# Optimization experiments

Measured on AMD Instinct MI355X. Metric: run time of the kernel, lower is better.

The kernel has to match this reference:

```python
import jax, jax.numpy as jnp
import numpy as np

B, T, E, H = 1, 4096, 768, 12
DH = E // H


def setup_inputs() -> dict:
    key = jax.random.key(0)
    ks = jax.random.split(key, 10)
    s = 0.02
    inp = {
        "queries": jax.random.normal(ks[0], (B, T, E), jnp.float32),
        "values": jax.random.normal(ks[1], (B, T, E), jnp.float32),
        # causal mask (1 = keep, 0 = masked), matches masked_fill(mask == 0, -1e9)
        "mask": jnp.tril(jnp.ones((T, T), jnp.int32))[None, None, :, :],
        "Wq": jax.random.normal(ks[2], (E, E), jnp.float32) * s,
        "bq": jnp.zeros((E,), jnp.float32),
        "Wk": jax.random.normal(ks[3], (E, E), jnp.float32) * s,
        "bk": jnp.zeros((E,), jnp.float32),
        "Wv": jax.random.normal(ks[4], (E, E), jnp.float32) * s,
        "bv": jnp.zeros((E,), jnp.float32),
        "Wo": jax.random.normal(ks[5], (E, E), jnp.float32) * s,
        "bo": jnp.zeros((E,), jnp.float32),
    }
    return inp


def _split_heads(x):
    # [B,T,E] -> [B,H,T,DH]
    return x.reshape(B, T, H, DH).transpose(0, 2, 1, 3)


def reference(queries, values, mask, Wq, bq, Wk, bk, Wv, bv, Wo, bo):
    # torch nn.Linear: y = x @ W.T + b
    q = _split_heads(queries @ Wq.T + bq)
    k = _split_heads(values @ Wk.T + bk)
    v = _split_heads(values @ Wv.T + bv)
    scale = 1.0 / np.sqrt(DH).astype(np.float32)
    logits = jnp.einsum("bhqd,bhkd->bhqk", q, k) * scale  # [B,H,T,T]
    logits = jnp.where(mask == 0, jnp.float32(-1e9), logits)
    probs = jax.nn.softmax(logits, axis=-1)
    ctx = jnp.einsum("bhqk,bhkd->bhqd", probs, v)  # [B,H,T,DH]
    ctx = ctx.transpose(0, 2, 1, 3).reshape(B, T, E)
    return ctx @ Wo.T + bo
```

## Files before the change

kernel.cpp:

```cpp
#include <hip/hip_runtime.h>
#include <hip/hip_bf16.h>


typedef __hip_bfloat16 bf16;
typedef __attribute__((ext_vector_type(8))) short short8;
typedef __attribute__((ext_vector_type(4))) short short4v;
typedef __attribute__((ext_vector_type(4))) float f32x4;

#define TSEQ 4096
#define NHEAD 12
#define DHEAD 64
#define EMB 768

#if defined(__HIP_DEVICE_COMPILE__)
#define MFMA16(a, b, c) __builtin_amdgcn_mfma_f32_16x16x16bf16_1k(a, b, c, 0, 0, 0)
#else
#define MFMA16(a, b, c) (c)
#endif

typedef const __attribute__((address_space(1))) unsigned int* gptr_t;
typedef __attribute__((address_space(3))) unsigned int* lptr_t;

__device__ __forceinline__ void load_lds16(const void* g, void* l) {
    __builtin_amdgcn_global_load_lds((gptr_t)g, (lptr_t)l, 16, 0, 0);
}

__device__ __forceinline__ float b2f(short s) {
    unsigned u = ((unsigned)(unsigned short)s) << 16;
    float f;
    __builtin_memcpy(&f, &u, 4);
    return f;
}

__device__ __forceinline__ short f2bs(float f) {
    bf16 h = __float2bfloat16(f);
    short s;
    __builtin_memcpy(&s, &h, 2);
    return s;
}

struct CvtJob { const float* src; bf16* dst; int n; };
struct CvtArgs { CvtJob j[6]; };

__global__ __launch_bounds__(256) void cvt_kernel(CvtArgs a) {
    const CvtJob jb = a.j[blockIdx.y];
    const int i = (blockIdx.x * 256 + threadIdx.x) * 8;
    if (i >= jb.n) return;
    const float4 x0 = *(const float4*)(jb.src + i);
    const float4 x1 = *(const float4*)(jb.src + i + 4);
    bf16 tmp[8];
    tmp[0] = __float2bfloat16(x0.x); tmp[1] = __float2bfloat16(x0.y);
    tmp[2] = __float2bfloat16(x0.z); tmp[3] = __float2bfloat16(x0.w);
    tmp[4] = __float2bfloat16(x1.x); tmp[5] = __float2bfloat16(x1.y);
    tmp[6] = __float2bfloat16(x1.z); tmp[7] = __float2bfloat16(x1.w);
    *(short8*)(jb.dst + i) = *(const short8*)tmp;
}

__device__ __forceinline__ void gemm128(
    const bf16* __restrict__ A, const bf16* __restrict__ W,
    const float* __restrict__ bias,
    bf16* __restrict__ outb, float* __restrict__ outf,
    const int mode, const float scale, const int m0, const int n0,
    bf16* sA, bf16* sB)
{
    const int tid  = threadIdx.x;
    const int lane = tid & 63;
    const int wave = tid >> 6;
    const int wr = wave >> 1, wc = wave & 1;
    const int lg = lane >> 4, lr = lane & 15;

    f32x4 acc[4][4];
#pragma unroll
    for (int m = 0; m < 4; ++m)
#pragma unroll
        for (int n = 0; n < 4; ++n)
            acc[m][n] = (f32x4){0.f, 0.f, 0.f, 0.f};

    for (int k0 = 0; k0 < EMB; k0 += 64) {
        if (k0) __syncthreads();
#pragma unroll
        for (int is = 0; is < 4; ++is) {
            const int chunk = is * 256 + tid;
            const int row = chunk >> 3;
            const int csw = (chunk & 7) ^ (row & 7);
            load_lds16(A + (size_t)(m0 + row) * EMB + k0 + csw * 8,
                       sA + is * 2048 + wave * 512);
            load_lds16(W + (size_t)(n0 + row) * EMB + k0 + csw * 8,
                       sB + is * 2048 + wave * 512);
        }
        __syncthreads();

        short8 af[4][2], bfv[4][2];
#pragma unroll
        for (int m = 0; m < 4; ++m)
#pragma unroll
            for (int kk = 0; kk < 2; ++kk) {
                const int row = wr * 64 + m * 16 + lr;
                const int cc = (kk * 4 + lg) ^ (row & 7);
                af[m][kk] = *(const short8*)(sA + row * 64 + cc * 8);
            }
#pragma unroll
        for (int n = 0; n < 4; ++n)
#pragma unroll
            for (int kk = 0; kk < 2; ++kk) {
                const int row = wc * 64 + n * 16 + lr;
                const int cc = (kk * 4 + lg) ^ (row & 7);
                bfv[n][kk] = *(const short8*)(sB + row * 64 + cc * 8);
            }
#pragma unroll
        for (int kk = 0; kk < 2; ++kk)
#pragma unroll
            for (int m = 0; m < 4; ++m)
#pragma unroll
                for (int n = 0; n < 4; ++n)
                    acc[m][n] = __builtin_amdgcn_mfma_f32_16x16x32_bf16(
                        af[m][kk], bfv[n][kk], acc[m][n], 0, 0, 0);
    }

#pragma unroll
    for (int n = 0; n < 4; ++n) {
        const int o = n0 + wc * 64 + n * 16 + lr;
        const float bv = bias[o];
#pragma unroll
        for (int m = 0; m < 4; ++m) {
            const int tbase = m0 + wr * 64 + m * 16 + lg * 4;
#pragma unroll
            for (int r = 0; r < 4; ++r) {
                const float v = (acc[m][n][r] + bv) * scale;
                const int t = tbase + r;
                if (mode == 0)
                    outb[(size_t)(o >> 6) * TSEQ * DHEAD + (size_t)t * DHEAD + (o & 63)] =
                        __float2bfloat16(v);
                else if (mode == 1)
                    outb[(size_t)(o >> 6) * DHEAD * TSEQ + (size_t)(o & 63) * TSEQ + t] =
                        __float2bfloat16(v);
                else
                    outf[(size_t)t * EMB + o] = v;
            }
        }
    }
}

struct QkvArgs {
    const bf16 *xq, *xv, *Wq, *Wk, *Wv;
    const float *bq, *bk, *bv;
    bf16 *qo, *ko, *vto;
};

__global__ __launch_bounds__(256) void qkv_gemm(QkvArgs a) {
    __shared__ __attribute__((aligned(16))) bf16 sA[128 * 64];
    __shared__ __attribute__((aligned(16))) bf16 sB[128 * 64];
    const int z = blockIdx.z;
    const bf16* A = (z == 0) ? a.xq : a.xv;
    const bf16* W = (z == 0) ? a.Wq : (z == 1 ? a.Wk : a.Wv);
    const float* b = (z == 0) ? a.bq : (z == 1 ? a.bk : a.bv);
    bf16* o = (z == 0) ? a.qo : (z == 1 ? a.ko : a.vto);
    const int mode = (z == 2) ? 1 : 0;
    const float scale = (z == 0) ? 0.18033688011112042f : 1.0f;
    gemm128(A, W, b, o, nullptr, mode, scale, blockIdx.x * 128, blockIdx.y * 128, sA, sB);
}

__global__ __launch_bounds__(256) void out_gemm(
    const bf16* __restrict__ ctx, const bf16* __restrict__ Wo,
    const float* __restrict__ bo, float* __restrict__ out)
{
    __shared__ __attribute__((aligned(16))) bf16 sA[128 * 64];
    __shared__ __attribute__((aligned(16))) bf16 sB[128 * 64];
    gemm128(ctx, Wo, bo, nullptr, out, 2, 1.0f, blockIdx.x * 128, blockIdx.y * 128, sA, sB);
}

struct AttnState {
    f32x4 O[4];
    float m, l;
};

__device__ __forceinline__ void stage_tile(
    const bf16* __restrict__ Kh, const bf16* __restrict__ Vh,
    bf16* sK, bf16* sV, const int kv0, const int tid)
{
    const int wave = tid >> 6;
#pragma unroll
    for (int is = 0; is < 2; ++is) {
        const int chunk = is * 256 + tid;
        const int row = chunk >> 3;
        const int csw = (chunk & 7) ^ (row & 7);
        load_lds16(Kh + (size_t)(kv0 + row) * DHEAD + csw * 8,
                   sK + is * 2048 + wave * 512);
        load_lds16(Vh + (size_t)row * TSEQ + kv0 + csw * 8,
                   sV + is * 2048 + wave * 512);
    }
}

__device__ __forceinline__ void attn_tile(
    const bf16* sK, const bf16* sV,
    const short8 (&qf)[2], AttnState& st,
    const int kv0, const int qw, const int lane)
{
    const int lg = lane >> 4, lr = lane & 15;
    if (kv0 > qw + 15) return;

    f32x4 s[4];
#pragma unroll
    for (int n = 0; n < 4; ++n) s[n] = (f32x4){0.f, 0.f, 0.f, 0.f};
    short8 kf[4][2];
#pragma unroll
    for (int n = 0; n < 4; ++n)
#pragma unroll
        for (int kk = 0; kk < 2; ++kk) {
            const int row = n * 16 + lr;
            const int cc = (kk * 4 + lg) ^ (row & 7);
            kf[n][kk] = *(const short8*)(sK + row * 64 + cc * 8);
        }
#pragma unroll
    for (int kk = 0; kk < 2; ++kk)
#pragma unroll
        for (int n = 0; n < 4; ++n)
            s[n] = __builtin_amdgcn_mfma_f32_16x16x32_bf16(
                kf[n][kk], qf[kk], s[n], 0, 0, 0);

    if (kv0 + 63 > qw) {
        const int qi = qw + lr;
#pragma unroll
        for (int n = 0; n < 4; ++n) {
            const int kb = kv0 + n * 16 + lg * 4;
#pragma unroll
            for (int r = 0; r < 4; ++r)
                if (kb + r > qi) s[n][r] = -3.0e38f;
        }
    }

    float mx = s[0][0];
#pragma unroll
    for (int n = 0; n < 4; ++n)
#pragma unroll
        for (int r = 0; r < 4; ++r) mx = fmaxf(mx, s[n][r]);
    mx = fmaxf(mx, __shfl_xor(mx, 16));
    mx = fmaxf(mx, __shfl_xor(mx, 32));

    const float mn = fmaxf(st.m, mx);
    const float al = __builtin_amdgcn_exp2f(st.m - mn);
    st.m = mn;

    float rs = 0.f;
    short4v pq[4];
#pragma unroll
    for (int n = 0; n < 4; ++n) {
#pragma unroll
        for (int r = 0; r < 4; ++r) {
            const float p = __builtin_amdgcn_exp2f(s[n][r] - mn);
            s[n][r] = p;
            rs += p;
        }
        pq[n][0] = f2bs(s[n][0]); pq[n][1] = f2bs(s[n][1]);
        pq[n][2] = f2bs(s[n][2]); pq[n][3] = f2bs(s[n][3]);
    }
    rs += __shfl_xor(rs, 16);
    rs += __shfl_xor(rs, 32);
    st.l = st.l * al + rs;

#pragma unroll
    for (int nd = 0; nd < 4; ++nd)
#pragma unroll
        for (int r = 0; r < 4; ++r)
            st.O[nd][r] *= al;

#pragma unroll
    for (int nd = 0; nd < 4; ++nd) {
        const int row = nd * 16 + lr;
        f32x4 o = st.O[nd];
#pragma unroll
        for (int n = 0; n < 4; ++n) {
            const int c16 = (n * 2 + (lg >> 1)) ^ (row & 7);
            const short4v va = *(const short4v*)(sV + row * 64 + c16 * 8 + (lg & 1) * 4);
            o = MFMA16(va, pq[n], o);
        }
        st.O[nd] = o;
    }
}

__global__ __launch_bounds__(256, 4) void attn_kernel(
    const bf16* __restrict__ Q, const bf16* __restrict__ K,
    const bf16* __restrict__ VT, bf16* __restrict__ Opart,
    float* __restrict__ ml, const int nch)
{
    __shared__ __attribute__((aligned(16))) bf16 sK0[64 * 64];
    __shared__ __attribute__((aligned(16))) bf16 sK1[64 * 64];
    __shared__ __attribute__((aligned(16))) bf16 sV0[64 * 64];
    __shared__ __attribute__((aligned(16))) bf16 sV1[64 * 64];

    const int tid  = threadIdx.x;
    const int lane = tid & 63;
    const int wave = tid >> 6;
    const int lg = lane >> 4, lr = lane & 15;
    const int h  = blockIdx.z;
    const int c  = blockIdx.y;
    const int bx = gridDim.x - 1 - blockIdx.x;
    const int q0 = bx * 64;
    const int qw = q0 + wave * 16;

    const bf16* Qh = Q  + (size_t)h * TSEQ * DHEAD;
    const bf16* Kh = K  + (size_t)h * TSEQ * DHEAD;
    const bf16* Vh = VT + (size_t)h * DHEAD * TSEQ;

    const int S  = bx + 1;
    const int t0 = (c * S) / nch;
    const int t1 = ((c + 1) * S) / nch;

    short8 qf[2];
#pragma unroll
    for (int kk = 0; kk < 2; ++kk)
        qf[kk] = *(const short8*)(Qh + (size_t)(qw + lr) * DHEAD + kk * 32 + lg * 8);

    AttnState st;
#pragma unroll
    for (int nd = 0; nd < 4; ++nd) st.O[nd] = (f32x4){0.f, 0.f, 0.f, 0.f};
    st.m = -3.0e38f; st.l = 0.f;

    if (t0 < t1) stage_tile(Kh, Vh, sK0, sV0, t0 * 64, tid);
    __syncthreads();

    int it = t0;
    while (it < t1) {
        if (it + 1 < t1) stage_tile(Kh, Vh, sK1, sV1, (it + 1) * 64, tid);
        attn_tile(sK0, sV0, qf, st, it * 64, qw, lane);
        __syncthreads();
        ++it;
        if (it >= t1) break;
        if (it + 1 < t1) stage_tile(Kh, Vh, sK0, sV0, (it + 1) * 64, tid);
        attn_tile(sK1, sV1, qf, st, it * 64, qw, lane);
        __syncthreads();
        ++it;
    }

    const int u = (h * 64 + bx) * nch + c;
    bf16* op = Opart + (size_t)u * 4096;
    float* mlp = ml + (size_t)u * 128;
    const int q = wave * 16 + lr;
#pragma unroll
    for (int nd = 0; nd < 4; ++nd) {
        short4v ov;
        ov[0] = f2bs(st.O[nd][0]); ov[1] = f2bs(st.O[nd][1]);
        ov[2] = f2bs(st.O[nd][2]); ov[3] = f2bs(st.O[nd][3]);
        *(short4v*)(op + q * 64 + nd * 16 + lg * 4) = ov;
    }
    if (lg == 0) {
        mlp[q] = st.m;
        mlp[64 + q] = st.l;
    }
}

__global__ __launch_bounds__(256) void combine_kernel(
    const bf16* __restrict__ Opart, const float* __restrict__ ml,
    bf16* __restrict__ ctx, const int nch)
{
    const int h  = blockIdx.y;
    const int bx = blockIdx.x;
    const int tid = threadIdx.x;
    const int row = tid >> 2;
    const int dp  = (tid & 3) * 16;
    const int ub = (h * 64 + bx) * nch;

    float m[4], l[4], w[4];
    float M = -3.0e38f;
    for (int c = 0; c < nch; ++c) {
        m[c] = ml[(size_t)(ub + c) * 128 + row];
        l[c] = ml[(size_t)(ub + c) * 128 + 64 + row];
        M = fmaxf(M, m[c]);
    }
    float L = 0.f;
    for (int c = 0; c < nch; ++c) {
        w[c] = __builtin_amdgcn_exp2f(m[c] - M);
        L += l[c] * w[c];
    }
    const float invL = 1.0f / L;

    float acc[16];
#pragma unroll
    for (int i = 0; i < 16; ++i) acc[i] = 0.f;
    for (int c = 0; c < nch; ++c) {
        const bf16* op = Opart + ((size_t)(ub + c) * 64 + row) * 64 + dp;
        const short8 v0 = *(const short8*)op;
        const short8 v1 = *(const short8*)(op + 8);
#pragma unroll
        for (int i = 0; i < 8; ++i) acc[i] += w[c] * b2f(v0[i]);
#pragma unroll
        for (int i = 0; i < 8; ++i) acc[8 + i] += w[c] * b2f(v1[i]);
    }
    bf16 outv[16];
#pragma unroll
    for (int i = 0; i < 16; ++i) outv[i] = __float2bfloat16(acc[i] * invL);
    const int t = bx * 64 + row;
    bf16* dst = ctx + (size_t)t * EMB + h * DHEAD + dp;
    *(short8*)dst = *(const short8*)outv;
    *(short8*)(dst + 8) = *(const short8*)(outv + 8);
}

extern "C" void kernel_launch(void* const* d_in, const int* in_sizes, int n_in,
                              void* d_out, int out_size, void* d_ws, size_t ws_size,
                              hipStream_t stream) {
    const float* queries = (const float*)d_in[0];
    const float* values  = (const float*)d_in[1];
    const float* Wq = (const float*)d_in[3];
    const float* bq = (const float*)d_in[4];
    const float* Wk = (const float*)d_in[5];
    const float* bk = (const float*)d_in[6];
    const float* Wv = (const float*)d_in[7];
    const float* bv = (const float*)d_in[8];
    const float* Wo = (const float*)d_in[9];
    const float* bo = (const float*)d_in[10];
    float* out = (float*)d_out;

    const size_t NTE = (size_t)TSEQ * EMB;
    const size_t WSZ = (size_t)EMB * EMB;
    bf16* ws  = (bf16*)d_ws;
    bf16* qb  = ws;
    bf16* vb  = qb + NTE;
    bf16* wqb = vb + NTE;
    bf16* wkb = wqb + WSZ;
    bf16* wvb = wkb + WSZ;
    bf16* wob = wvb + WSZ;
    bf16* qh  = wob + WSZ;
    bf16* kh  = qh + NTE;
    bf16* vth = kh + NTE;
    bf16* ctx = qb;

    const size_t fixed_elems = 5 * NTE + 4 * WSZ;
    int nch = 4;
    {
        const size_t units = (size_t)NHEAD * (TSEQ / 64) * nch;
        const size_t need = fixed_elems * 2 + units * 4096 * 2 + units * 128 * 4;
        if (ws_size < need) nch = 1;
    }
    const size_t units = (size_t)NHEAD * (TSEQ / 64) * nch;
    bf16* opart = ws + fixed_elems;
    float* ml = (float*)(opart + units * 4096);

    CvtArgs ca;
    ca.j[0] = {queries, qb,  (int)NTE};
    ca.j[1] = {values,  vb,  (int)NTE};
    ca.j[2] = {Wq,      wqb, (int)WSZ};
    ca.j[3] = {Wk,      wkb, (int)WSZ};
    ca.j[4] = {Wv,      wvb, (int)WSZ};
    ca.j[5] = {Wo,      wob, (int)WSZ};
    cvt_kernel<<<dim3((NTE + 2047) / 2048, 6), 256, 0, stream>>>(ca);

    QkvArgs a{qb, vb, wqb, wkb, wvb, bq, bk, bv, qh, kh, vth};
    qkv_gemm<<<dim3(TSEQ / 128, EMB / 128, 3), 256, 0, stream>>>(a);
    attn_kernel<<<dim3(TSEQ / 64, nch, NHEAD), 256, 0, stream>>>(qh, kh, vth, opart, ml, nch);
    combine_kernel<<<dim3(TSEQ / 64, NHEAD), 256, 0, stream>>>(opart, ml, ctx, nch);
    out_gemm<<<dim3(TSEQ / 128, EMB / 128), 256, 0, stream>>>(ctx, wob, bo, out);
}
```

Before: 135.3 us.

## Process 32 query rows per wave to reuse K/V fragments across two row blocks

```diff
diff --git a/kernel.cpp b/kernel.cpp
--- a/kernel.cpp
+++ b/kernel.cpp
@@ -170,8 +170,8 @@
 }
 
 struct AttnState {
-    f32x4 O[4];
-    float m, l;
+    f32x4 O[2][4];
+    float m[2], l[2];
 };
 
 __device__ __forceinline__ void stage_tile(
@@ -191,91 +191,99 @@
     }
 }
 
-__device__ __forceinline__ void attn_tile(
+__device__ __forceinline__ void attn_tile32(
     const bf16* sK, const bf16* sV,
-    const short8 (&qf)[2], AttnState& st,
+    const short8 (&qf)[2][2], AttnState& st,
     const int kv0, const int qw, const int lane)
 {
     const int lg = lane >> 4, lr = lane & 15;
-    if (kv0 > qw + 15) return;
-
-    f32x4 s[4];
-#pragma unroll
-    for (int n = 0; n < 4; ++n) s[n] = (f32x4){0.f, 0.f, 0.f, 0.f};
-    short8 kf[4][2];
-#pragma unroll
-    for (int n = 0; n < 4; ++n)
-#pragma unroll
-        for (int kk = 0; kk < 2; ++kk) {
-            const int row = n * 16 + lr;
-            const int cc = (kk * 4 + lg) ^ (row & 7);
-            kf[n][kk] = *(const short8*)(sK + row * 64 + cc * 8);
-        }
-#pragma unroll
-    for (int kk = 0; kk < 2; ++kk)
+    if (kv0 > qw + 31) return;
+
+    short4v pq[2][4];
+#pragma unroll
+    for (int mm = 0; mm < 2; ++mm) {
+        f32x4 s[4];
+#pragma unroll
+        for (int n = 0; n < 4; ++n) s[n] = (f32x4){0.f, 0.f, 0.f, 0.f};
+        short8 kf[4][2];
 #pragma unroll
         for (int n = 0; n < 4; ++n)
-            s[n] = __builtin_amdgcn_mfma_f32_16x16x32_bf16(
-                kf[n][kk], qf[kk], s[n], 0, 0, 0);
-
-    if (kv0 + 63 > qw) {
-        const int qi = qw + lr;
+#pragma unroll
+            for (int kk = 0; kk < 2; ++kk) {
+                const int row = n * 16 + lr;
+                const int cc = (kk * 4 + lg) ^ (row & 7);
+                kf[n][kk] = *(const short8*)(sK + row * 64 + cc * 8);
+            }
+        __builtin_amdgcn_s_setprio(1);
+#pragma unroll
+        for (int kk = 0; kk < 2; ++kk)
+#pragma unroll
+            for (int n = 0; n < 4; ++n)
+                s[n] = __builtin_amdgcn_mfma_f32_16x16x32_bf16(
+                    kf[n][kk], qf[mm][kk], s[n], 0, 0, 0);
+        __builtin_amdgcn_s_setprio(0);
+
+        const int qm = qw + mm * 16;
+        if (kv0 + 63 > qm) {
+            const int qi = qm + lr;
+#pragma unroll
+            for (int n = 0; n < 4; ++n) {
+                const int kb = kv0 + n * 16 + lg * 4;
+#pragma unroll
+                for (int r = 0; r < 4; ++r)
+                    if (kb + r > qi) s[n][r] = -3.0e38f;
+            }
+        }
+
+        float mx = s[0][0];
+#pragma unroll
+        for (int n = 0; n < 4; ++n)
+#pragma unroll
+            for (int r = 0; r < 4; ++r) mx = fmaxf(mx, s[n][r]);
+        mx = fmaxf(mx, __shfl_xor(mx, 16));
+        mx = fmaxf(mx, __shfl_xor(mx, 32));
+
+        const float mn = fmaxf(st.m[mm], mx);
+        const float al = __builtin_amdgcn_exp2f(st.m[mm] - mn);
+        st.m[mm] = mn;
+
+        float rs = 0.f;
 #pragma unroll
         for (int n = 0; n < 4; ++n) {
-            const int kb = kv0 + n * 16 + lg * 4;
+            float p0 = __builtin_amdgcn_exp2f(s[n][0] - mn);
+            float p1 = __builtin_amdgcn_exp2f(s[n][1] - mn);
+            float p2 = __builtin_amdgcn_exp2f(s[n][2] - mn);
+            float p3 = __builtin_amdgcn_exp2f(s[n][3] - mn);
+            rs += (p0 + p1) + (p2 + p3);
+            pq[mm][n][0] = f2bs(p0); pq[mm][n][1] = f2bs(p1);
+            pq[mm][n][2] = f2bs(p2); pq[mm][n][3] = f2bs(p3);
+        }
+        rs += __shfl_xor(rs, 16);
+        rs += __shfl_xor(rs, 32);
+        st.l[mm] = st.l[mm] * al + rs;
+
+#pragma unroll
+        for (int nd = 0; nd < 4; ++nd)
 #pragma unroll
             for (int r = 0; r < 4; ++r)
-                if (kb + r > qi) s[n][r] = -3.0e38f;
-        }
-    }
-
-    float mx = s[0][0];
-#pragma unroll
-    for (int n = 0; n < 4; ++n)
-#pragma unroll
-        for (int r = 0; r < 4; ++r) mx = fmaxf(mx, s[n][r]);
-    mx = fmaxf(mx, __shfl_xor(mx, 16));
-    mx = fmaxf(mx, __shfl_xor(mx, 32));
-
-    const float mn = fmaxf(st.m, mx);
-    const float al = __builtin_amdgcn_exp2f(st.m - mn);
-    st.m = mn;
-
-    float rs = 0.f;
-    short4v pq[4];
-#pragma unroll
-    for (int n = 0; n < 4; ++n) {
-#pragma unroll
-        for (int r = 0; r < 4; ++r) {
-            const float p = __builtin_amdgcn_exp2f(s[n][r] - mn);
-            s[n][r] = p;
-            rs += p;
-        }
-        pq[n][0] = f2bs(s[n][0]); pq[n][1] = f2bs(s[n][1]);
-        pq[n][2] = f2bs(s[n][2]); pq[n][3] = f2bs(s[n][3]);
-    }
-    rs += __shfl_xor(rs, 16);
-    rs += __shfl_xor(rs, 32);
-    st.l = st.l * al + rs;
-
-#pragma unroll
-    for (int nd = 0; nd < 4; ++nd)
-#pragma unroll
-        for (int r = 0; r < 4; ++r)
-            st.O[nd][r] *= al;
-
+                st.O[mm][nd][r] *= al;
+    }
+
+    __builtin_amdgcn_s_setprio(1);
 #pragma unroll
     for (int nd = 0; nd < 4; ++nd) {
         const int row = nd * 16 + lr;
-        f32x4 o = st.O[nd];
+        f32x4 o0 = st.O[0][nd], o1 = st.O[1][nd];
 #pragma unroll
         for (int n = 0; n < 4; ++n) {
             const int c16 = (n * 2 + (lg >> 1)) ^ (row & 7);
             const short4v va = *(const short4v*)(sV + row * 64 + c16 * 8 + (lg & 1) * 4);
-            o = MFMA16(va, pq[n], o);
-        }
-        st.O[nd] = o;
-    }
+            o0 = MFMA16(va, pq[0][n], o0);
+            o1 = MFMA16(va, pq[1][n], o1);
+        }
+        st.O[0][nd] = o0; st.O[1][nd] = o1;
+    }
+    __builtin_amdgcn_s_setprio(0);
 }
 
 __global__ __launch_bounds__(256, 4) void attn_kernel(
@@ -295,26 +303,31 @@
     const int h  = blockIdx.z;
     const int c  = blockIdx.y;
     const int bx = gridDim.x - 1 - blockIdx.x;
-    const int q0 = bx * 64;
-    const int qw = q0 + wave * 16;
+    const int q0 = bx * 128;
+    const int qw = q0 + wave * 32;
 
     const bf16* Qh = Q  + (size_t)h * TSEQ * DHEAD;
     const bf16* Kh = K  + (size_t)h * TSEQ * DHEAD;
     const bf16* Vh = VT + (size_t)h * DHEAD * TSEQ;
 
-    const int S  = bx + 1;
+    const int S  = 2 * bx + 2;
     const int t0 = (c * S) / nch;
     const int t1 = ((c + 1) * S) / nch;
 
-    short8 qf[2];
-#pragma unroll
-    for (int kk = 0; kk < 2; ++kk)
-        qf[kk] = *(const short8*)(Qh + (size_t)(qw + lr) * DHEAD + kk * 32 + lg * 8);
+    short8 qf[2][2];
+#pragma unroll
+    for (int mm = 0; mm < 2; ++mm)
+#pragma unroll
+        for (int kk = 0; kk < 2; ++kk)
+            qf[mm][kk] = *(const short8*)(Qh + (size_t)(qw + mm * 16 + lr) * DHEAD + kk * 32 + lg * 8);
 
     AttnState st;
 #pragma unroll
-    for (int nd = 0; nd < 4; ++nd) st.O[nd] = (f32x4){0.f, 0.f, 0.f, 0.f};
-    st.m = -3.0e38f; st.l = 0.f;
+    for (int mm = 0; mm < 2; ++mm) {
+#pragma unroll
+        for (int nd = 0; nd < 4; ++nd) st.O[mm][nd] = (f32x4){0.f, 0.f, 0.f, 0.f};
+        st.m[mm] = -3.0e38f; st.l[mm] = 0.f;
+    }
 
     if (t0 < t1) stage_tile(Kh, Vh, sK0, sV0, t0 * 64, tid);
     __syncthreads();
@@ -322,30 +335,34 @@
     int it = t0;
     while (it < t1) {
         if (it + 1 < t1) stage_tile(Kh, Vh, sK1, sV1, (it + 1) * 64, tid);
-        attn_tile(sK0, sV0, qf, st, it * 64, qw, lane);
+        attn_tile32(sK0, sV0, qf, st, it * 64, qw, lane);
         __syncthreads();
         ++it;
         if (it >= t1) break;
         if (it + 1 < t1) stage_tile(Kh, Vh, sK0, sV0, (it + 1) * 64, tid);
-        attn_tile(sK1, sV1, qf, st, it * 64, qw, lane);
+        attn_tile32(sK1, sV1, qf, st, it * 64, qw, lane);
         __syncthreads();
         ++it;
     }
 
-    const int u = (h * 64 + bx) * nch + c;
-    bf16* op = Opart + (size_t)u * 4096;
-    float* mlp = ml + (size_t)u * 128;
-    const int q = wave * 16 + lr;
-#pragma unroll
-    for (int nd = 0; nd < 4; ++nd) {
-        short4v ov;
-        ov[0] = f2bs(st.O[nd][0]); ov[1] = f2bs(st.O[nd][1]);
-        ov[2] = f2bs(st.O[nd][2]); ov[3] = f2bs(st.O[nd][3]);
-        *(short4v*)(op + q * 64 + nd * 16 + lg * 4) = ov;
-    }
-    if (lg == 0) {
-        mlp[q] = st.m;
-        mlp[64 + q] = st.l;
+#pragma unroll
+    for (int mm = 0; mm < 2; ++mm) {
+        const int rowblk = wave * 32 + mm * 16;
+        const int u = (h * 64 + bx * 2 + (rowblk >> 6)) * nch + c;
+        bf16* op = Opart + (size_t)u * 4096;
+        float* mlp = ml + (size_t)u * 128;
+        const int q = (rowblk & 63) + lr;
+#pragma unroll
+        for (int nd = 0; nd < 4; ++nd) {
+            short4v ov;
+            ov[0] = f2bs(st.O[mm][nd][0]); ov[1] = f2bs(st.O[mm][nd][1]);
+            ov[2] = f2bs(st.O[mm][nd][2]); ov[3] = f2bs(st.O[mm][nd][3]);
+            *(short4v*)(op + q * 64 + nd * 16 + lg * 4) = ov;
+        }
+        if (lg == 0) {
+            mlp[q] = st.m[mm];
+            mlp[64 + q] = st.l[mm];
+        }
     }
 }
 
@@ -446,7 +463,7 @@
 
     QkvArgs a{qb, vb, wqb, wkb, wvb, bq, bk, bv, qh, kh, vth};
     qkv_gemm<<<dim3(TSEQ / 128, EMB / 128, 3), 256, 0, stream>>>(a);
-    attn_kernel<<<dim3(TSEQ / 64, nch, NHEAD), 256, 0, stream>>>(qh, kh, vth, opart, ml, nch);
+    attn_kernel<<<dim3(TSEQ / 128, nch, NHEAD), 256, 0, stream>>>(qh, kh, vth, opart, ml, nch);
     combine_kernel<<<dim3(TSEQ / 64, NHEAD), 256, 0, stream>>>(opart, ml, ctx, nch);
     out_gemm<<<dim3(TSEQ / 128, EMB / 128), 256, 0, stream>>>(ctx, wob, bo, out);
 }
```

Result: slower. 242.8 us (+79.5%).
